# Kernel optimization log

Measured on AMD Instinct MI355X. Metric: run time of the kernel, lower is better.

The kernel has to match this reference:

```python
import jax, jax.numpy as jnp
import numpy as np

B = 4096      # batch
D = 64        # state_dim
H = 512       # hidden_dim


def setup_inputs() -> dict:
    key = jax.random.key(0)
    ks = jax.random.split(key, 16)

    def init(k, shape, fan_in):
        return jax.random.normal(k, shape, dtype=jnp.float32) / np.float32(np.sqrt(fan_in))

    mu = jax.random.normal(ks[0], (B, D), dtype=jnp.float32)
    sigma_diag = 0.1 * jax.random.uniform(ks[1], (B, D), dtype=jnp.float32) + 0.01
    states = jnp.concatenate([mu, sigma_diag], axis=1)  # [B, 2D]

    return {
        "t": jnp.float32(0.5),
        "states": states,
        # dynamics net: tanh MLP D -> H -> H -> D
        "W1": init(ks[2], (H, D), D), "b1": jnp.zeros((H,), jnp.float32),
        "W2": init(ks[3], (H, H), H), "b2": jnp.zeros((H,), jnp.float32),
        "W3": init(ks[4], (D, H), H), "b3": jnp.zeros((D,), jnp.float32),
        # process-noise net: tanh MLP D -> H -> H -> D, softplus head (diagonal Q)
        "V1": init(ks[5], (H, D), D), "c1": jnp.zeros((H,), jnp.float32),
        "V2": init(ks[6], (H, H), H), "c2": jnp.zeros((H,), jnp.float32),
        "V3": init(ks[7], (D, H), H), "c3": jnp.zeros((D,), jnp.float32),
    }


def reference(t, states, W1, b1, W2, b2, W3, b3, V1, c1, V2, c2, V3, c3):
    # UPN ODE function, diagonal-covariance path.
    mu = states[:, :D]          # [B, D]
    sigma_diag = states[:, D:]  # [B, D]

    # dynamics MLP forward (t is an autonomous-system placeholder, unused)
    h1 = jnp.tanh(mu @ W1.T + b1)   # [B, H]
    h2 = jnp.tanh(h1 @ W2.T + b2)   # [B, H]
    mu_drift = h2 @ W3.T + b3       # [B, D]

    # analytic batched Jacobian of the tanh MLP: J = W3 diag(1-h2^2) W2 diag(1-h1^2) W1
    d1 = 1.0 - h1 * h1              # [B, H]
    d2 = 1.0 - h2 * h2              # [B, H]
    inner = jnp.einsum('hk,bk,kd->bhd', W2, d1, W1)   # [B, H, D]
    J = jnp.einsum('oh,bh,bhd->bod', W3, d2, inner)   # [B, D, D]
    J_diag = jnp.diagonal(J, axis1=1, axis2=2)        # [B, D]

    # process-noise net: diagonal Q, softplus ensures positivity
    g1 = jnp.tanh(mu @ V1.T + c1)
    g2 = jnp.tanh(g1 @ V2.T + c2)
    Q_diag = jax.nn.softplus(g2 @ V3.T + c3)          # [B, D]

    sigma_drift = 2.0 * J_diag * sigma_diag + Q_diag  # [B, D]
    return jnp.concatenate([mu_drift, sigma_drift], axis=1)  # [B, 2D]
```

## Files before the change

### kernel.cpp

```cpp
#include <hip/hip_runtime.h>
#include <hip/hip_bf16.h>

#define BB 4096
#define DD 64
#define HH 512

typedef __hip_bfloat16 bf16;
typedef _Float16 f16;
typedef __attribute__((ext_vector_type(8))) short bf16x8;
typedef __attribute__((ext_vector_type(8))) _Float16 f16x8;
typedef __attribute__((ext_vector_type(4))) float f32x4;

__device__ __forceinline__ float bf2f(bf16 x) { return __bfloat162float(x); }
__device__ __forceinline__ float u16tof(unsigned short u) {
  union { unsigned int i; float f; } v; v.i = ((unsigned int)u) << 16; return v.f;
}
#define BC8(p) __builtin_bit_cast(bf16x8, *(const uint4*)(p))
#define BCH8(p) __builtin_bit_cast(f16x8, *(const uint4*)(p))


__global__ __launch_bounds__(256) void cvt_weights(
    const float* __restrict__ W2, const float* __restrict__ V2,
    const float* __restrict__ W1, const float* __restrict__ V1,
    const float* __restrict__ W3, const float* __restrict__ V3,
    bf16* __restrict__ W2bf, bf16* __restrict__ V2bf, f16* __restrict__ W1Th,
    bf16* __restrict__ W1bf, bf16* __restrict__ V1bf,
    bf16* __restrict__ W3bf, bf16* __restrict__ V3bf, f16* __restrict__ W2h) {
  int blk = blockIdx.x, t = threadIdx.x;
  if (blk < 512) {
    const float* src = (blk < 256) ? W2 : V2;
    bf16* dst = (blk < 256) ? W2bf : V2bf;
    int i = ((blk & 255) * 256 + t) * 4;
    float4 v = *(const float4*)(src + i);
    bf16 o[4] = {__float2bfloat16(v.x), __float2bfloat16(v.y),
                 __float2bfloat16(v.z), __float2bfloat16(v.w)};
    *(uint2*)(dst + i) = *(uint2*)o;
  } else if (blk < 544) {
    int e = (blk - 512) * 1024 + t * 4;
    int d = e >> 9, k0 = e & 511;
    f16 o[4];
#pragma unroll
    for (int j = 0; j < 4; ++j) o[j] = (f16)W1[(size_t)(k0 + j) * 64 + d];
    *(uint2*)(W1Th + e) = *(uint2*)o;
  } else if (blk < 672) {
    int which = (blk - 544) >> 5;
    int local = (blk - 544) & 31;
    const float* src = (which == 0) ? W1 : (which == 1) ? V1 : (which == 2) ? W3 : V3;
    bf16* dst = (which == 0) ? W1bf : (which == 1) ? V1bf : (which == 2) ? W3bf : V3bf;
    int i = (local * 256 + t) * 4;
    float4 v = *(const float4*)(src + i);
    bf16 o[4] = {__float2bfloat16(v.x), __float2bfloat16(v.y),
                 __float2bfloat16(v.z), __float2bfloat16(v.w)};
    *(uint2*)(dst + i) = *(uint2*)o;
  } else {
    int i = ((blk - 672) * 256 + t) * 4;
    float4 v = *(const float4*)(W2 + i);
    f16 o[4] = {(f16)v.x, (f16)v.y, (f16)v.z, (f16)v.w};
    *(uint2*)(W2h + i) = *(uint2*)o;
  }
}

__global__ __launch_bounds__(256) void fwd(
    const float* __restrict__ states,
    const bf16* __restrict__ W1bf, const float* __restrict__ b1,
    const bf16* __restrict__ W2bf, const float* __restrict__ b2,
    const bf16* __restrict__ W3bf, const float* __restrict__ b3,
    const bf16* __restrict__ V1bf, const float* __restrict__ c1,
    const bf16* __restrict__ V2bf, const float* __restrict__ c2,
    const bf16* __restrict__ V3bf, const float* __restrict__ c3,
    bf16* __restrict__ Xbf, bf16* __restrict__ Ybf, float* __restrict__ out) {
  __shared__ __align__(16) bf16 mus[16 * 72];
  __shared__ __align__(16) bf16 Xres[16 * 520];
  __shared__ __align__(16) bf16 Bs[128 * 72];
  __shared__ __align__(16) bf16 Ych[16 * 136];
  const int bt = blockIdx.x * 16;
  const int path = blockIdx.y;
  const bf16* Wa = path ? V1bf : W1bf;
  const float* ba = path ? c1 : b1;
  const bf16* Wb = path ? V2bf : W2bf;
  const float* bbv = path ? c2 : b2;
  const bf16* Wc = path ? V3bf : W3bf;
  const float* bcv = path ? c3 : b3;
  const int t = threadIdx.x;
  const int lane = t & 63;
  const int w = t >> 6;
  const int c = lane & 15, q = lane >> 4;

  if (t < 128) {
    int row = t >> 3, cg = (t & 7) * 8;
    bf16 o[8];
#pragma unroll
    for (int j = 0; j < 8; j += 4) {
      float4 v = *(const float4*)(states + (size_t)(bt + row) * 128 + cg + j);
      o[j] = __float2bfloat16(v.x); o[j + 1] = __float2bfloat16(v.y);
      o[j + 2] = __float2bfloat16(v.z); o[j + 3] = __float2bfloat16(v.w);
    }
    *(uint4*)(mus + row * 72 + cg) = *(const uint4*)o;
  }
  __syncthreads();

  for (int nch = 0; nch < 4; ++nch) {
    if (nch) __syncthreads();
#pragma unroll
    for (int i = 0; i < 4; ++i) {
      int g = t + i * 256;
      int row = g >> 3, kb = (g & 7) * 8;
      *(uint4*)(Bs + row * 72 + kb) =
          *(const uint4*)(Wa + (size_t)(nch * 128 + row) * 64 + kb);
    }
    __syncthreads();
    f32x4 acc1[2] = {};
#pragma unroll
    for (int s = 0; s < 2; ++s) {
      bf16x8 af = BC8(mus + c * 72 + s * 32 + q * 8);
#pragma unroll
      for (int nt = 0; nt < 2; ++nt) {
        bf16x8 bfr = BC8(Bs + (w * 32 + nt * 16 + c) * 72 + s * 32 + q * 8);
        acc1[nt] = __builtin_amdgcn_mfma_f32_16x16x32_bf16(af, bfr, acc1[nt], 0, 0, 0);
      }
    }
#pragma unroll
    for (int nt = 0; nt < 2; ++nt) {
      int col = nch * 128 + w * 32 + nt * 16 + c;
      float bias = ba[col];
#pragma unroll
      for (int r = 0; r < 4; ++r) {
        int row = q * 4 + r;
        float x = tanhf(acc1[nt][r] + bias);
        Xres[row * 520 + col] = __float2bfloat16(x);
        if (!path) Xbf[(size_t)(bt + row) * HH + col] = __float2bfloat16(x);
      }
    }
  }
  __syncthreads();

  f32x4 acc3 = {};
  for (int hch = 0; hch < 4; ++hch) {
    f32x4 acc2[2] = {};
    for (int kc = 0; kc < 8; ++kc) {
      __syncthreads();
#pragma unroll
      for (int i = 0; i < 4; ++i) {
        int g = t + i * 256;
        int row = g >> 3, kb = (g & 7) * 8;
        *(uint4*)(Bs + row * 72 + kb) =
            *(const uint4*)(Wb + (size_t)(hch * 128 + row) * HH + kc * 64 + kb);
      }
      __syncthreads();
#pragma unroll
      for (int s = 0; s < 2; ++s) {
        bf16x8 af = BC8(Xres + c * 520 + kc * 64 + s * 32 + q * 8);
#pragma unroll
        for (int nt = 0; nt < 2; ++nt) {
          bf16x8 bfr = BC8(Bs + (w * 32 + nt * 16 + c) * 72 + s * 32 + q * 8);
          acc2[nt] = __builtin_amdgcn_mfma_f32_16x16x32_bf16(af, bfr, acc2[nt], 0, 0, 0);
        }
      }
    }
    __syncthreads();
#pragma unroll
    for (int nt = 0; nt < 2; ++nt) {
      int hl = w * 32 + nt * 16 + c;
      int h = hch * 128 + hl;
      float bias = bbv[h];
#pragma unroll
      for (int r = 0; r < 4; ++r) {
        int row = q * 4 + r;
        float y = tanhf(acc2[nt][r] + bias);
        Ych[row * 136 + hl] = __float2bfloat16(y);
        if (!path) Ybf[(size_t)(bt + row) * HH + h] = __float2bfloat16(y);
      }
    }
    __syncthreads();
#pragma unroll
    for (int s3 = 0; s3 < 4; ++s3) {
      bf16x8 bf3 = BC8(Wc + (size_t)(w * 16 + c) * HH + hch * 128 + s3 * 32 + q * 8);
      bf16x8 af3 = BC8(Ych + c * 136 + s3 * 32 + q * 8);
      acc3 = __builtin_amdgcn_mfma_f32_16x16x32_bf16(af3, bf3, acc3, 0, 0, 0);
    }
  }
  {
    int o = w * 16 + c;
    float bias = bcv[o];
#pragma unroll
    for (int r = 0; r < 4; ++r) {
      int row = q * 4 + r;
      float v = acc3[r] + bias;
      if (path) {
        v = fmaxf(v, 0.0f) + log1pf(expf(-fabsf(v)));
        out[(size_t)(bt + row) * 128 + 64 + o] = v;
      } else {
        out[(size_t)(bt + row) * 128 + o] = v;
      }
    }
  }
}

__global__ __launch_bounds__(256, 4) void k4_gemm(
    const bf16* __restrict__ Xbf, const bf16* __restrict__ Ybf,
    const f16* __restrict__ W1Th, const f16* __restrict__ W2h,
    const float* __restrict__ W3, float* __restrict__ Jpart) {
  __shared__ __align__(16) f16 smem[2 * 128 * 72];
  __shared__ __align__(16) f16 d1h[2 * 512];
  __shared__ __align__(16) float d2f[2 * 128];
  f16* As = smem;
  f16* Bs = smem + 128 * 72;
  const int bt = blockIdx.x;
  const int h0 = blockIdx.y * 128;
  const int t = threadIdx.x;
  const int lane = t & 63;
  const int w = t >> 6, wm = w & 1, wn = w >> 1;
  const int c = lane & 15, q = lane >> 4;

#pragma unroll
  for (int i = 0; i < 4; ++i) {
    int e = t + i * 256;
    float x = bf2f(Xbf[(size_t)(bt * 2 + (e >> 9)) * HH + (e & 511)]);
    d1h[e] = (f16)(1.0f - x * x);
  }
  {
    float y = bf2f(Ybf[(size_t)(bt * 2 + (t >> 7)) * HH + h0 + (t & 127)]);
    d2f[t] = 1.0f - y * y;
  }
  __syncthreads();

  f32x4 acc[4][4] = {};
  for (int kc = 0; kc < 8; ++kc) {
#pragma unroll
    for (int i = 0; i < 4; ++i) {
      int g = t + i * 256;
      int m = g >> 3, kb = (g & 7) * 8;
      int bb = m >> 6, dl = m & 63;
      f16x8 w1v = BCH8(W1Th + (size_t)dl * HH + kc * 64 + kb);
      f16x8 d1v = BCH8(d1h + bb * 512 + kc * 64 + kb);
      f16x8 av = d1v * w1v;
      *(uint4*)(As + m * 72 + kb) = __builtin_bit_cast(uint4, av);
      *(uint4*)(Bs + m * 72 + kb) =
          *(const uint4*)(W2h + (size_t)(h0 + m) * HH + kc * 64 + kb);
    }
    __syncthreads();
#pragma unroll
    for (int s = 0; s < 2; ++s) {
      f16x8 af[4], bfr[4];
#pragma unroll
      for (int mt = 0; mt < 4; ++mt)
        af[mt] = BCH8(As + (wm * 64 + mt * 16 + c) * 72 + s * 32 + q * 8);
#pragma unroll
      for (int nt = 0; nt < 4; ++nt)
        bfr[nt] = BCH8(Bs + (wn * 64 + nt * 16 + c) * 72 + s * 32 + q * 8);
#pragma unroll
      for (int mt = 0; mt < 4; ++mt)
#pragma unroll
        for (int nt = 0; nt < 4; ++nt)
          acc[mt][nt] = __builtin_amdgcn_mfma_f32_16x16x32_f16(
              af[mt], bfr[nt], acc[mt][nt], 0, 0, 0);
    }
    __syncthreads();
  }

  f16* w3s = As;
  float* red = (float*)Bs;
#pragma unroll
  for (int i = 0; i < 8; ++i) {
    int e = (t + i * 256) * 4;
    int dl = e >> 7, hl = e & 127;
    float4 v = *(const float4*)(W3 + (size_t)dl * HH + h0 + hl);
    f16 o[4] = {(f16)v.x, (f16)v.y, (f16)v.z, (f16)v.w};
    *(uint2*)(w3s + dl * 136 + hl) = *(uint2*)o;
  }
  __syncthreads();

#pragma unroll
  for (int mt = 0; mt < 4; ++mt) {
#pragma unroll
    for (int r = 0; r < 4; ++r) {
      int m = wm * 64 + mt * 16 + q * 4 + r;
      int bb = m >> 6, dl = m & 63;
      float v = 0.f;
#pragma unroll
      for (int nt = 0; nt < 4; ++nt) {
        int n = wn * 64 + nt * 16 + c;
        v += acc[mt][nt][r] * d2f[bb * 128 + n] * (float)w3s[dl * 136 + n];
      }
      v += __shfl_xor(v, 1);
      v += __shfl_xor(v, 2);
      v += __shfl_xor(v, 4);
      v += __shfl_xor(v, 8);
      if (c == 0) red[wn * 128 + m] = v;
    }
  }
  __syncthreads();
  if (t < 128) {
    float J = red[t] + red[128 + t];
    Jpart[(size_t)blockIdx.y * (BB * 64) + (size_t)bt * 128 + t] = J;
  }
}

__global__ __launch_bounds__(256) void combine(
    const float* __restrict__ Jpart, const float* __restrict__ states,
    float* __restrict__ out) {
  int idx = blockIdx.x * 256 + threadIdx.x;
  int b = idx >> 6, d = idx & 63;
  const int plane = BB * 64;
  float J = Jpart[idx] + Jpart[plane + idx] + Jpart[2 * plane + idx] +
            Jpart[3 * plane + idx];
  float sig = states[(size_t)b * 128 + 64 + d];
  float qd = out[(size_t)b * 128 + 64 + d];
  out[(size_t)b * 128 + 64 + d] = 2.0f * J * sig + qd;
}

extern "C" void kernel_launch(void* const* d_in, const int* in_sizes, int n_in,
                              void* d_out, int out_size, void* d_ws, size_t ws_size,
                              hipStream_t stream) {
  const float* states = (const float*)d_in[1];
  const float* W1 = (const float*)d_in[2];
  const float* b1 = (const float*)d_in[3];
  const float* W2 = (const float*)d_in[4];
  const float* b2 = (const float*)d_in[5];
  const float* W3 = (const float*)d_in[6];
  const float* b3 = (const float*)d_in[7];
  const float* V1 = (const float*)d_in[8];
  const float* c1 = (const float*)d_in[9];
  const float* V2 = (const float*)d_in[10];
  const float* c2 = (const float*)d_in[11];
  const float* V3 = (const float*)d_in[12];
  const float* c3 = (const float*)d_in[13];
  float* out = (float*)d_out;

  bf16* Xbf = (bf16*)d_ws;
  bf16* Ybf = Xbf + (size_t)BB * HH;
  bf16* W2bf = Ybf + (size_t)BB * HH;
  bf16* V2bf = W2bf + (size_t)HH * HH;
  bf16* W1bf = V2bf + (size_t)HH * HH;
  bf16* V1bf = W1bf + (size_t)HH * DD;
  bf16* W3bf = V1bf + (size_t)HH * DD;
  bf16* V3bf = W3bf + (size_t)DD * HH;
  f16* W1Th = (f16*)(V3bf + (size_t)DD * HH);
  f16* W2h = W1Th + (size_t)DD * HH;
  float* Jpart = (float*)(W2h + (size_t)HH * HH);

  cvt_weights<<<dim3(928), 256, 0, stream>>>(W2, V2, W1, V1, W3, V3,
                                             W2bf, V2bf, W1Th, W1bf, V1bf,
                                             W3bf, V3bf, W2h);
  fwd<<<dim3(256, 2), 256, 0, stream>>>(states, W1bf, b1, W2bf, b2, W3bf, b3,
                                        V1bf, c1, V2bf, c2, V3bf, c3,
                                        Xbf, Ybf, out);
  k4_gemm<<<dim3(2048, 4), 256, 0, stream>>>(Xbf, Ybf, W1Th, W2h, W3, Jpart);
  combine<<<dim3(1024), 256, 0, stream>>>(Jpart, states, out);
}
```

Before: 313.9 us.

## Restructure Jacobian GEMM with async LDS triple-buffering, swizzled weights, larger tiles

Weights W2 and W1 are pre-converted to fp16 in an XOR-swizzled, k-chunked layout so each stage can be copied straight into LDS with global_load_lds. A three-buffer pipeline with explicit vmcnt waits overlaps those copies with MFMA work. The Jacobian GEMM now uses 512-thread blocks covering 4 batch rows by 256 hidden units, which halves the grid and the number of partial J planes. The d1 scaling moves into registers just before each MFMA, and the W3/d2 epilogue is reorganised. In exchange the kernel needs 128KB of LDS and 128 accumulator registers per thread, which limits occupancy.

Measured after the change: 320.8 us. 1.02x slower.

```diff
diff --git a/kernel.cpp b/kernel.cpp
--- a/kernel.cpp
+++ b/kernel.cpp
@@ -18,14 +18,21 @@
 #define BC8(p) __builtin_bit_cast(bf16x8, *(const uint4*)(p))
 #define BCH8(p) __builtin_bit_cast(f16x8, *(const uint4*)(p))
 
+__device__ __forceinline__ void gl16(const void* g, void* l) {
+  __builtin_amdgcn_global_load_lds((__attribute__((address_space(1))) void*)g,
+                                   (__attribute__((address_space(3))) void*)l,
+                                   16, 0, 0);
+}
+
 
 __global__ __launch_bounds__(256) void cvt_weights(
     const float* __restrict__ W2, const float* __restrict__ V2,
     const float* __restrict__ W1, const float* __restrict__ V1,
     const float* __restrict__ W3, const float* __restrict__ V3,
-    bf16* __restrict__ W2bf, bf16* __restrict__ V2bf, f16* __restrict__ W1Th,
+    bf16* __restrict__ W2bf, bf16* __restrict__ V2bf,
     bf16* __restrict__ W1bf, bf16* __restrict__ V1bf,
-    bf16* __restrict__ W3bf, bf16* __restrict__ V3bf, f16* __restrict__ W2h) {
+    bf16* __restrict__ W3bf, bf16* __restrict__ V3bf,
+    f16* __restrict__ W2sw, f16* __restrict__ W1sw) {
   int blk = blockIdx.x, t = threadIdx.x;
   if (blk < 512) {
     const float* src = (blk < 256) ? W2 : V2;
@@ -35,16 +42,28 @@
     bf16 o[4] = {__float2bfloat16(v.x), __float2bfloat16(v.y),
                  __float2bfloat16(v.z), __float2bfloat16(v.w)};
     *(uint2*)(dst + i) = *(uint2*)o;
-  } else if (blk < 544) {
-    int e = (blk - 512) * 1024 + t * 4;
-    int d = e >> 9, k0 = e & 511;
-    f16 o[4];
-#pragma unroll
-    for (int j = 0; j < 4; ++j) o[j] = (f16)W1[(size_t)(k0 + j) * 64 + d];
-    *(uint2*)(W1Th + e) = *(uint2*)o;
-  } else if (blk < 672) {
-    int which = (blk - 544) >> 5;
-    int local = (blk - 544) & 31;
+  } else if (blk < 640) {
+    int uid = (blk - 512) * 256 + t;
+    int kc = uid >> 12, rem = uid & 4095;
+    int h = rem >> 3, u = rem & 7;
+    const float* src = W2 + (size_t)h * HH + kc * 64 + u * 8;
+    float4 a = *(const float4*)src;
+    float4 b = *(const float4*)(src + 4);
+    f16 o[8] = {(f16)a.x, (f16)a.y, (f16)a.z, (f16)a.w,
+                (f16)b.x, (f16)b.y, (f16)b.z, (f16)b.w};
+    *(uint4*)(W2sw + (size_t)((kc * 512 + h) * 8 + (u ^ (h & 7))) * 8) = *(uint4*)o;
+  } else if (blk < 656) {
+    int uid = (blk - 640) * 256 + t;
+    int kc = uid >> 9, rem = uid & 511;
+    int dl = rem >> 3, u = rem & 7;
+    f16 o[8];
+#pragma unroll
+    for (int e = 0; e < 8; ++e)
+      o[e] = (f16)W1[(size_t)(kc * 64 + u * 8 + e) * DD + dl];
+    *(uint4*)(W1sw + (size_t)((kc * 64 + dl) * 8 + (u ^ (dl & 7))) * 8) = *(uint4*)o;
+  } else {
+    int which = (blk - 656) >> 5;
+    int local = (blk - 656) & 31;
     const float* src = (which == 0) ? W1 : (which == 1) ? V1 : (which == 2) ? W3 : V3;
     bf16* dst = (which == 0) ? W1bf : (which == 1) ? V1bf : (which == 2) ? W3bf : V3bf;
     int i = (local * 256 + t) * 4;
@@ -52,11 +71,6 @@
     bf16 o[4] = {__float2bfloat16(v.x), __float2bfloat16(v.y),
                  __float2bfloat16(v.z), __float2bfloat16(v.w)};
     *(uint2*)(dst + i) = *(uint2*)o;
-  } else {
-    int i = ((blk - 672) * 256 + t) * 4;
-    float4 v = *(const float4*)(W2 + i);
-    f16 o[4] = {(f16)v.x, (f16)v.y, (f16)v.z, (f16)v.w};
-    *(uint2*)(W2h + i) = *(uint2*)o;
   }
 }
 
@@ -196,103 +210,167 @@
   }
 }
 
-__global__ __launch_bounds__(256, 4) void k4_gemm(
+#define LDSB(buf) ((buf) * 32768)
+#define LDSA(buf) (98304 + (buf) * 8192)
+#define LDSD1 122880
+#define LDSD2 126976
+#define LDSRED 98304
+
+#define STAGE(kc_, buf_) do {                                                  \
+    const char* gb_ = (const char*)W2sw + ((size_t)(kc_) * 512 + h0) * 128;    \
+    char* lb_ = (char*)lds + LDSB(buf_);                                       \
+    gl16(gb_ + t * 16, lb_ + t * 16);                                          \
+    gl16(gb_ + 8192 + t * 16, lb_ + 8192 + t * 16);                            \
+    gl16(gb_ + 16384 + t * 16, lb_ + 16384 + t * 16);                          \
+    gl16(gb_ + 24576 + t * 16, lb_ + 24576 + t * 16);                          \
+    gl16((const char*)W1sw + (kc_) * 8192 + t * 16,                            \
+         (char*)lds + LDSA(buf_) + t * 16);                                    \
+  } while (0)
+
+__global__ __launch_bounds__(512, 2) void k4_gemm(
     const bf16* __restrict__ Xbf, const bf16* __restrict__ Ybf,
-    const f16* __restrict__ W1Th, const f16* __restrict__ W2h,
+    const f16* __restrict__ W1sw, const f16* __restrict__ W2sw,
     const float* __restrict__ W3, float* __restrict__ Jpart) {
-  __shared__ __align__(16) f16 smem[2 * 128 * 72];
-  __shared__ __align__(16) f16 d1h[2 * 512];
-  __shared__ __align__(16) float d2f[2 * 128];
-  f16* As = smem;
-  f16* Bs = smem + 128 * 72;
+  __shared__ __align__(16) char lds[131072];
   const int bt = blockIdx.x;
-  const int h0 = blockIdx.y * 128;
+  const int h0 = blockIdx.y * 256;
   const int t = threadIdx.x;
   const int lane = t & 63;
-  const int w = t >> 6, wm = w & 1, wn = w >> 1;
+  const int w = t >> 6;
   const int c = lane & 15, q = lane >> 4;
-
-#pragma unroll
-  for (int i = 0; i < 4; ++i) {
-    int e = t + i * 256;
-    float x = bf2f(Xbf[(size_t)(bt * 2 + (e >> 9)) * HH + (e & 511)]);
-    d1h[e] = (f16)(1.0f - x * x);
-  }
+  const int wr = w >> 2, wc = w & 3;
+  const int b0 = bt * 4;
+
   {
-    float y = bf2f(Ybf[(size_t)(bt * 2 + (t >> 7)) * HH + h0 + (t & 127)]);
-    d2f[t] = 1.0f - y * y;
-  }
-  __syncthreads();
-
-  f32x4 acc[4][4] = {};
+    int e = t * 4, j = e >> 9, k = e & 511;
+    ushort4 xv = *(const ushort4*)((const unsigned short*)Xbf +
+                                   (size_t)(b0 + j) * HH + k);
+    f16 o[4];
+    float x;
+    x = u16tof(xv.x); o[0] = (f16)(1.f - x * x);
+    x = u16tof(xv.y); o[1] = (f16)(1.f - x * x);
+    x = u16tof(xv.z); o[2] = (f16)(1.f - x * x);
+    x = u16tof(xv.w); o[3] = (f16)(1.f - x * x);
+    *(uint2*)(lds + LDSD1 + e * 2) = *(uint2*)o;
+  }
+  {
+    int e = t * 2, j = e >> 8, n = e & 255;
+    ushort2 yv = *(const ushort2*)((const unsigned short*)Ybf +
+                                   (size_t)(b0 + j) * HH + h0 + n);
+    float y0 = u16tof(yv.x), y1 = u16tof(yv.y);
+    float2 d2v = {1.f - y0 * y0, 1.f - y1 * y1};
+    *(float2*)(lds + LDSD2 + e * 4) = d2v;
+  }
+  __syncthreads();
+
+  STAGE(0, 0);
+  STAGE(1, 1);
+
+  const int cj = c & 7;
+  const int j16_0 = ((0 + q) ^ cj) * 16;
+  const int j16_1 = ((4 + q) ^ cj) * 16;
+  const int arow = c * 128;
+  const int brow = (wc * 64 + c) * 128;
+  const int d1base = LDSD1 + wr * 2048 + q * 16;
+
+  f32x4 acc[8][4] = {};
+
+#pragma unroll
   for (int kc = 0; kc < 8; ++kc) {
+    const int buf = kc % 3;
+    if (kc < 7) { asm volatile("s_waitcnt vmcnt(5)\n\ts_barrier" ::: "memory"); }
+    else        { asm volatile("s_waitcnt vmcnt(0)\n\ts_barrier" ::: "memory"); }
+    if (kc < 6) STAGE(kc + 2, (kc + 2) % 3);
+
+    f16x8 bfr[4][2], w1f[4][2], d1v[2][2];
+#pragma unroll
+    for (int nt = 0; nt < 4; ++nt) {
+      bfr[nt][0] = BCH8(lds + LDSB(buf) + brow + nt * 2048 + j16_0);
+      bfr[nt][1] = BCH8(lds + LDSB(buf) + brow + nt * 2048 + j16_1);
+    }
 #pragma unroll
     for (int i = 0; i < 4; ++i) {
-      int g = t + i * 256;
-      int m = g >> 3, kb = (g & 7) * 8;
-      int bb = m >> 6, dl = m & 63;
-      f16x8 w1v = BCH8(W1Th + (size_t)dl * HH + kc * 64 + kb);
-      f16x8 d1v = BCH8(d1h + bb * 512 + kc * 64 + kb);
-      f16x8 av = d1v * w1v;
-      *(uint4*)(As + m * 72 + kb) = __builtin_bit_cast(uint4, av);
-      *(uint4*)(Bs + m * 72 + kb) =
-          *(const uint4*)(W2h + (size_t)(h0 + m) * HH + kc * 64 + kb);
-    }
-    __syncthreads();
-#pragma unroll
-    for (int s = 0; s < 2; ++s) {
-      f16x8 af[4], bfr[4];
-#pragma unroll
-      for (int mt = 0; mt < 4; ++mt)
-        af[mt] = BCH8(As + (wm * 64 + mt * 16 + c) * 72 + s * 32 + q * 8);
-#pragma unroll
-      for (int nt = 0; nt < 4; ++nt)
-        bfr[nt] = BCH8(Bs + (wn * 64 + nt * 16 + c) * 72 + s * 32 + q * 8);
-#pragma unroll
-      for (int mt = 0; mt < 4; ++mt)
+      w1f[i][0] = BCH8(lds + LDSA(buf) + arow + i * 2048 + j16_0);
+      w1f[i][1] = BCH8(lds + LDSA(buf) + arow + i * 2048 + j16_1);
+    }
+#pragma unroll
+    for (int b = 0; b < 2; ++b) {
+      d1v[b][0] = BCH8(lds + d1base + b * 1024 + kc * 128);
+      d1v[b][1] = BCH8(lds + d1base + b * 1024 + kc * 128 + 64);
+    }
+    __builtin_amdgcn_s_setprio(1);
+#pragma unroll
+    for (int mt = 0; mt < 8; ++mt) {
+#pragma unroll
+      for (int s = 0; s < 2; ++s) {
+        f16x8 av = w1f[mt & 3][s] * d1v[mt >> 2][s];
 #pragma unroll
         for (int nt = 0; nt < 4; ++nt)
           acc[mt][nt] = __builtin_amdgcn_mfma_f32_16x16x32_f16(
-              af[mt], bfr[nt], acc[mt][nt], 0, 0, 0);
-    }
-    __syncthreads();
-  }
-
-  f16* w3s = As;
-  float* red = (float*)Bs;
+              av, bfr[nt][s], acc[mt][nt], 0, 0, 0);
+      }
+    }
+    __builtin_amdgcn_s_setprio(0);
+  }
+  __syncthreads();
+
 #pragma unroll
   for (int i = 0; i < 8; ++i) {
-    int e = (t + i * 256) * 4;
-    int dl = e >> 7, hl = e & 127;
-    float4 v = *(const float4*)(W3 + (size_t)dl * HH + h0 + hl);
-    f16 o[4] = {(f16)v.x, (f16)v.y, (f16)v.z, (f16)v.w};
-    *(uint2*)(w3s + dl * 136 + hl) = *(uint2*)o;
-  }
-  __syncthreads();
-
-#pragma unroll
-  for (int mt = 0; mt < 4; ++mt) {
+    int e = (t + i * 512) * 4;
+    int dl = e >> 8, col = e & 255;
+    float4 v = *(const float4*)(W3 + (size_t)dl * HH + h0 + col);
+    *(float*)(lds + ((col + 0) * 72 + dl) * 4) = v.x;
+    *(float*)(lds + ((col + 1) * 72 + dl) * 4) = v.y;
+    *(float*)(lds + ((col + 2) * 72 + dl) * 4) = v.z;
+    *(float*)(lds + ((col + 3) * 72 + dl) * 4) = v.w;
+  }
+  __syncthreads();
+
+  float d2r[2][4];
+#pragma unroll
+  for (int bh = 0; bh < 2; ++bh)
+#pragma unroll
+    for (int nt = 0; nt < 4; ++nt)
+      d2r[bh][nt] = *(const float*)(
+          lds + LDSD2 + ((wr * 2 + bh) * 256 + wc * 64 + nt * 16 + c) * 4);
+
+  float vsum[8][4] = {};
+#pragma unroll
+  for (int mt4 = 0; mt4 < 4; ++mt4)
+#pragma unroll
+    for (int nt = 0; nt < 4; ++nt) {
+      f32x4 w3v = *(const f32x4*)(
+          lds + ((wc * 64 + nt * 16 + c) * 72 + mt4 * 16 + q * 4) * 4);
+#pragma unroll
+      for (int bh = 0; bh < 2; ++bh) {
+        const int mt = bh * 4 + mt4;
+        float sc = d2r[bh][nt];
+#pragma unroll
+        for (int r = 0; r < 4; ++r)
+          vsum[mt][r] += acc[mt][nt][r] * w3v[r] * sc;
+      }
+    }
+
+#pragma unroll
+  for (int mt = 0; mt < 8; ++mt)
 #pragma unroll
     for (int r = 0; r < 4; ++r) {
-      int m = wm * 64 + mt * 16 + q * 4 + r;
-      int bb = m >> 6, dl = m & 63;
-      float v = 0.f;
-#pragma unroll
-      for (int nt = 0; nt < 4; ++nt) {
-        int n = wn * 64 + nt * 16 + c;
-        v += acc[mt][nt][r] * d2f[bb * 128 + n] * (float)w3s[dl * 136 + n];
-      }
+      float v = vsum[mt][r];
       v += __shfl_xor(v, 1);
       v += __shfl_xor(v, 2);
       v += __shfl_xor(v, 4);
       v += __shfl_xor(v, 8);
-      if (c == 0) red[wn * 128 + m] = v;
-    }
-  }
-  __syncthreads();
-  if (t < 128) {
-    float J = red[t] + red[128 + t];
-    Jpart[(size_t)blockIdx.y * (BB * 64) + (size_t)bt * 128 + t] = J;
+      if (c == 0)
+        *(float*)(lds + LDSRED +
+                  (wc * 256 + wr * 128 + mt * 16 + q * 4 + r) * 4) = v;
+    }
+  __syncthreads();
+  if (t < 256) {
+    float J = *(const float*)(lds + LDSRED + t * 4) +
+              *(const float*)(lds + LDSRED + (256 + t) * 4) +
+              *(const float*)(lds + LDSRED + (512 + t) * 4) +
+              *(const float*)(lds + LDSRED + (768 + t) * 4);
+    Jpart[(size_t)blockIdx.y * (BB * 64) + (size_t)bt * 256 + t] = J;
   }
 }
 
@@ -302,8 +380,7 @@
   int idx = blockIdx.x * 256 + threadIdx.x;
   int b = idx >> 6, d = idx & 63;
   const int plane = BB * 64;
-  float J = Jpart[idx] + Jpart[plane + idx] + Jpart[2 * plane + idx] +
-            Jpart[3 * plane + idx];
+  float J = Jpart[idx] + Jpart[plane + idx];
   float sig = states[(size_t)b * 128 + 64 + d];
   float qd = out[(size_t)b * 128 + 64 + d];
   out[(size_t)b * 128 + 64 + d] = 2.0f * J * sig + qd;
@@ -335,16 +412,16 @@
   bf16* V1bf = W1bf + (size_t)HH * DD;
   bf16* W3bf = V1bf + (size_t)HH * DD;
   bf16* V3bf = W3bf + (size_t)DD * HH;
-  f16* W1Th = (f16*)(V3bf + (size_t)DD * HH);
-  f16* W2h = W1Th + (size_t)DD * HH;
-  float* Jpart = (float*)(W2h + (size_t)HH * HH);
-
-  cvt_weights<<<dim3(928), 256, 0, stream>>>(W2, V2, W1, V1, W3, V3,
-                                             W2bf, V2bf, W1Th, W1bf, V1bf,
-                                             W3bf, V3bf, W2h);
+  f16* W1sw = (f16*)(V3bf + (size_t)DD * HH);
+  f16* W2sw = W1sw + (size_t)DD * HH;
+  float* Jpart = (float*)(W2sw + (size_t)HH * HH);
+
+  cvt_weights<<<dim3(784), 256, 0, stream>>>(W2, V2, W1, V1, W3, V3,
+                                             W2bf, V2bf, W1bf, V1bf,
+                                             W3bf, V3bf, W2sw, W1sw);
   fwd<<<dim3(256, 2), 256, 0, stream>>>(states, W1bf, b1, W2bf, b2, W3bf, b3,
                                         V1bf, c1, V2bf, c2, V3bf, c3,
                                         Xbf, Ybf, out);
-  k4_gemm<<<dim3(2048, 4), 256, 0, stream>>>(Xbf, Ybf, W1Th, W2h, W3, Jpart);
+  k4_gemm<<<dim3(1024, 2), 512, 0, stream>>>(Xbf, Ybf, W1sw, W2sw, W3, Jpart);
   combine<<<dim3(1024), 256, 0, stream>>>(Jpart, states, out);
 }
```
